# Performance work log

Hardware: AMD Instinct MI355X
Metric: run time of the kernel (lower is better)

The kernel has to match this reference:

```python
import jax, jax.numpy as jnp
import numpy as np

N_NODES = 50000
N_GENES = 256
N_EDGES = 800000
NUM_ITERATIONS = 10  # init_kwargs: num_iterations
SPARSITY = 0.3       # fraction of nonzero entries in expression matrix


def setup_inputs() -> dict:
    key = jax.random.key(0)
    k1, k2, k3, k4 = jax.random.split(key, 4)
    vals = jax.random.uniform(k1, (N_NODES, N_GENES), dtype=jnp.float32)
    keep = jax.random.uniform(k2, (N_NODES, N_GENES)) < SPARSITY
    x = jnp.where(keep, vals, 0.0)
    edge_index = jax.random.randint(k3, (2, N_EDGES), 0, N_NODES, dtype=jnp.int64)
    edge_weight = jax.random.uniform(k4, (N_EDGES,), dtype=jnp.float32)
    return {"x": x, "edge_index": edge_index, "edge_weight": edge_weight}


def reference(x, edge_index, edge_weight):
    # FeaturePropagation with mask=True, max_imputation_per_cell=None,
    # early_stopping=False: iterate x <- A @ x, then clamp known (nonzero)
    # entries back to their original values.
    n = x.shape[0]
    dst = edge_index[0]  # sparse COO row indices
    src = edge_index[1]  # sparse COO col indices
    orig = x
    known = x != 0

    def step(h, _):
        # SpMM: out[dst] += w * h[src]   (torch.sparse.mm(adj, x))
        msgs = edge_weight[:, None] * h[src]              # [E, G]
        h = jax.ops.segment_sum(msgs, dst, num_segments=n)  # [N, G]
        h = jnp.where(known, orig, h)  # reset known entries
        return h, None

    out, _ = jax.lax.scan(step, x, None, length=NUM_ITERATIONS)
    return out
```

## Files before the change

### kernel.cpp

```cpp
#include <hip/hip_runtime.h>

#define N_NODES 50000
#define N_GENES 256
#define N_EDGES 800000
#define NUM_ITERS 10
#define SCAN_BLK 1024
#define N_SCAN_BLKS ((N_NODES + SCAN_BLK - 1) / SCAN_BLK)

#define SLICE_G 128
#define N_SLICES 2
#define PROP_GRID 25000

typedef unsigned short u16;
struct u16x4 { u16 x, y, z, w; };

static __device__ __forceinline__ float bf2f(u16 b) {
    return __uint_as_float(((unsigned)b) << 16);
}
static __device__ __forceinline__ u16 f2bf(float f) {
    unsigned u = __float_as_uint(f);
    return (u16)((u + 0x7fffu + ((u >> 16) & 1u)) >> 16);
}


__global__ void hist_kernel(const int* __restrict__ dst, int* __restrict__ counts) {
    int e = blockIdx.x * blockDim.x + threadIdx.x;
    if (e < N_EDGES) atomicAdd(&counts[dst[e]], 1);
}

__global__ __launch_bounds__(SCAN_BLK) void scan1_kernel(
        const int* __restrict__ counts, int* __restrict__ offs,
        int* __restrict__ bsums) {
    int i = blockIdx.x * SCAN_BLK + threadIdx.x;
    int lane = threadIdx.x & 63, wid = threadIdx.x >> 6;
    int v = (i < N_NODES) ? counts[i] : 0;
    int x = v;
    #pragma unroll
    for (int o = 1; o < 64; o <<= 1) {
        int t = __shfl_up(x, o, 64);
        if (lane >= o) x += t;
    }
    __shared__ int wsum[16];
    if (lane == 63) wsum[wid] = x;
    __syncthreads();
    if (wid == 0 && lane < 16) {
        int y = wsum[lane];
        #pragma unroll
        for (int o = 1; o < 16; o <<= 1) {
            int t = __shfl_up(y, o, 64);
            if (lane >= o) y += t;
        }
        wsum[lane] = y;
    }
    __syncthreads();
    int pref = (wid > 0) ? wsum[wid - 1] : 0;
    int incl = x + pref;
    if (i < N_NODES) offs[i] = incl - v;
    if (threadIdx.x == SCAN_BLK - 1) bsums[blockIdx.x] = incl;
}

__global__ void scan2_kernel(const int* __restrict__ bsums,
                             int* __restrict__ bpref,
                             int* __restrict__ offs_total) {
    int lane = threadIdx.x;
    int v = (lane < N_SCAN_BLKS) ? bsums[lane] : 0;
    int x = v;
    #pragma unroll
    for (int o = 1; o < 64; o <<= 1) {
        int t = __shfl_up(x, o, 64);
        if (lane >= o) x += t;
    }
    if (lane < N_SCAN_BLKS) bpref[lane] = x - v;
    if (lane == 63) offs_total[0] = x;
}

__global__ __launch_bounds__(SCAN_BLK) void scan3_kernel(
        int* __restrict__ offs, const int* __restrict__ bpref,
        int* __restrict__ cursor) {
    int i = blockIdx.x * SCAN_BLK + threadIdx.x;
    if (i < N_NODES) {
        int o = offs[i] + bpref[blockIdx.x];
        offs[i] = o;
        cursor[i] = o;
    }
}

__global__ void scatter_kernel(const int* __restrict__ dst,
                               const int* __restrict__ src,
                               const float* __restrict__ w,
                               int* __restrict__ cursor,
                               int2* __restrict__ edges) {
    int e = blockIdx.x * blockDim.x + threadIdx.x;
    if (e < N_EDGES) {
        int d = dst[e];
        int p = atomicAdd(&cursor[d], 1);
        edges[p] = make_int2(src[e], __float_as_int(w[e]));
    }
}

__global__ __launch_bounds__(256) void cvt_slice_kernel(const float* __restrict__ x,
                                                        u16* __restrict__ xs) {
    int base = (blockIdx.x * blockDim.x + threadIdx.x) * 8;
    if (base >= N_NODES * N_GENES) return;
    int node = base >> 8;
    int gene = base & 255;
    int slice = gene >> 7;
    int g = gene & 127;
    float4 a = *reinterpret_cast<const float4*>(&x[base]);
    float4 b = *reinterpret_cast<const float4*>(&x[base + 4]);
    u16x4 r0 = { f2bf(a.x), f2bf(a.y), f2bf(a.z), f2bf(a.w) };
    u16x4 r1 = { f2bf(b.x), f2bf(b.y), f2bf(b.z), f2bf(b.w) };
    size_t o = (size_t)slice * (N_NODES * SLICE_G) + (size_t)node * SLICE_G + g;
    *reinterpret_cast<u16x4*>(&xs[o])     = r0;
    *reinterpret_cast<u16x4*>(&xs[o + 4]) = r1;
}


__global__ __launch_bounds__(256) void prop2_b(
        const u16* __restrict__ hin,
        const u16* __restrict__ xs,
        const int* __restrict__ offsets,
        const int2* __restrict__ edges,
        u16* __restrict__ out) {
    int b = blockIdx.x;
    int slice = ((b & 7) < 4) ? 0 : 1;
    int idx = (b >> 3) * 4 + (b & 3);
    int node = idx * 4 + (threadIdx.x >> 6);
    int lane = threadIdx.x & 63;
    int g2 = lane << 1;

    const u16* hs = hin + (size_t)slice * (N_NODES * SLICE_G);
    int beg = offsets[node], end = offsets[node + 1];
    float ax = 0.f, ay = 0.f;

    for (int base = beg; base < end; base += 64) {
        int cnt = end - base;
        if (cnt > 64) cnt = 64;
        int2 el = make_int2(0, 0);
        if (lane < cnt) {
            long long ev = __builtin_nontemporal_load(
                reinterpret_cast<const long long*>(&edges[base + lane]));
            el.x = (int)ev;
            el.y = (int)(ev >> 32);
        }

        int k = 0;
        for (; k + 8 <= cnt; k += 8) {
            int s[8]; float w[8]; unsigned p[8];
            #pragma unroll
            for (int j = 0; j < 8; ++j) {
                s[j] = __shfl(el.x, k + j);
                w[j] = __int_as_float(__shfl(el.y, k + j));
            }
            #pragma unroll
            for (int j = 0; j < 8; ++j)
                p[j] = *reinterpret_cast<const unsigned*>(&hs[(size_t)s[j] * SLICE_G + g2]);
            #pragma unroll
            for (int j = 0; j < 8; ++j) {
                ax += w[j] * bf2f((u16)p[j]);
                ay += w[j] * bf2f((u16)(p[j] >> 16));
            }
        }
        for (; k < cnt; ++k) {
            int   s = __shfl(el.x, k);
            float w = __int_as_float(__shfl(el.y, k));
            unsigned p = *reinterpret_cast<const unsigned*>(&hs[(size_t)s * SLICE_G + g2]);
            ax += w * bf2f((u16)p);
            ay += w * bf2f((u16)(p >> 16));
        }
    }

    size_t o = (size_t)slice * (N_NODES * SLICE_G) + (size_t)node * SLICE_G + g2;
    unsigned ox = __builtin_nontemporal_load(reinterpret_cast<const unsigned*>(&xs[o]));
    u16 b0 = (u16)(ox & 0xFFFFu), b1 = (u16)(ox >> 16);
    u16 r0 = b0 ? b0 : f2bf(ax);
    u16 r1 = b1 ? b1 : f2bf(ay);
    unsigned res = (unsigned)r0 | ((unsigned)r1 << 16);
    __builtin_nontemporal_store(res, reinterpret_cast<unsigned*>(&out[o]));
}

__global__ __launch_bounds__(256) void prop2_final(
        const u16* __restrict__ hin,
        const float* __restrict__ x,
        const int* __restrict__ offsets,
        const int2* __restrict__ edges,
        float* __restrict__ out) {
    int b = blockIdx.x;
    int slice = ((b & 7) < 4) ? 0 : 1;
    int idx = (b >> 3) * 4 + (b & 3);
    int node = idx * 4 + (threadIdx.x >> 6);
    int lane = threadIdx.x & 63;
    int g2 = lane << 1;

    const u16* hs = hin + (size_t)slice * (N_NODES * SLICE_G);
    int beg = offsets[node], end = offsets[node + 1];
    float ax = 0.f, ay = 0.f;

    for (int base = beg; base < end; base += 64) {
        int cnt = end - base;
        if (cnt > 64) cnt = 64;
        int2 el = make_int2(0, 0);
        if (lane < cnt) {
            long long ev = __builtin_nontemporal_load(
                reinterpret_cast<const long long*>(&edges[base + lane]));
            el.x = (int)ev;
            el.y = (int)(ev >> 32);
        }

        int k = 0;
        for (; k + 8 <= cnt; k += 8) {
            int s[8]; float w[8]; unsigned p[8];
            #pragma unroll
            for (int j = 0; j < 8; ++j) {
                s[j] = __shfl(el.x, k + j);
                w[j] = __int_as_float(__shfl(el.y, k + j));
            }
            #pragma unroll
            for (int j = 0; j < 8; ++j)
                p[j] = *reinterpret_cast<const unsigned*>(&hs[(size_t)s[j] * SLICE_G + g2]);
            #pragma unroll
            for (int j = 0; j < 8; ++j) {
                ax += w[j] * bf2f((u16)p[j]);
                ay += w[j] * bf2f((u16)(p[j] >> 16));
            }
        }
        for (; k < cnt; ++k) {
            int   s = __shfl(el.x, k);
            float w = __int_as_float(__shfl(el.y, k));
            unsigned p = *reinterpret_cast<const unsigned*>(&hs[(size_t)s * SLICE_G + g2]);
            ax += w * bf2f((u16)p);
            ay += w * bf2f((u16)(p >> 16));
        }
    }

    size_t xo = (size_t)node * N_GENES + slice * SLICE_G + g2;
    float2 o = *reinterpret_cast<const float2*>(&x[xo]);
    float2 r;
    r.x = (o.x != 0.f) ? o.x : ax;
    r.y = (o.y != 0.f) ? o.y : ay;
    *reinterpret_cast<float2*>(&out[xo]) = r;
}


static inline size_t align_up(size_t x, size_t a) { return (x + a - 1) & ~(a - 1); }

extern "C" void kernel_launch(void* const* d_in, const int* in_sizes, int n_in,
                              void* d_out, int out_size, void* d_ws, size_t ws_size,
                              hipStream_t stream) {
    const float* x    = (const float*)d_in[0];
    const int*   eidx = (const int*)d_in[1];
    const float* ew   = (const float*)d_in[2];
    float*       out  = (float*)d_out;

    const int* dst = eidx;
    const int* src = eidx + N_EDGES;

    char* ws = (char*)d_ws;
    size_t off = 0;
    u16*   xs      = (u16*) (ws + off); off += align_up((size_t)N_NODES * N_GENES * 2, 256);
    u16*   hsA     = (u16*) (ws + off); off += align_up((size_t)N_NODES * N_GENES * 2, 256);
    int2*  edges   = (int2*)(ws + off); off += align_up((size_t)N_EDGES * 8, 256);
    int*   counts  = (int*) (ws + off); off += align_up((size_t)N_NODES * 4, 256);
    int*   offsets = (int*) (ws + off); off += align_up((size_t)(N_NODES + 1) * 4, 256);
    int*   cursor  = (int*) (ws + off); off += align_up((size_t)N_NODES * 4, 256);
    int*   bsums   = (int*) (ws + off); off += align_up((size_t)N_SCAN_BLKS * 4, 256);
    int*   bpref   = (int*) (ws + off); off += align_up((size_t)N_SCAN_BLKS * 4, 256);
    (void)ws_size;

    u16* hsB = (u16*)d_out;

    hipMemsetAsync(counts, 0, (size_t)N_NODES * 4, stream);
    hist_kernel<<<(N_EDGES + 255) / 256, 256, 0, stream>>>(dst, counts);
    scan1_kernel<<<N_SCAN_BLKS, SCAN_BLK, 0, stream>>>(counts, offsets, bsums);
    scan2_kernel<<<1, 64, 0, stream>>>(bsums, bpref, &offsets[N_NODES]);
    scan3_kernel<<<N_SCAN_BLKS, SCAN_BLK, 0, stream>>>(offsets, bpref, cursor);
    scatter_kernel<<<(N_EDGES + 255) / 256, 256, 0, stream>>>(dst, src, ew, cursor, edges);
    cvt_slice_kernel<<<(N_NODES * N_GENES / 8 + 255) / 256, 256, 0, stream>>>(x, xs);

    const u16* hin = xs;
    for (int it = 0; it < NUM_ITERS - 1; ++it) {
        u16* hout = (it & 1) ? hsB : hsA;
        prop2_b<<<PROP_GRID, 256, 0, stream>>>(hin, xs, offsets, edges, hout);
        hin = hout;
    }
    prop2_final<<<PROP_GRID, 256, 0, stream>>>(hin, x, offsets, edges, out);
}
```

Before: 881.8 us.

## Split genes into eight 32-wide slices and pack edge metadata into 32 bits

After: 1.628 ms. 84.6% more time.

```diff
diff --git a/kernel.cpp b/kernel.cpp
--- a/kernel.cpp
+++ b/kernel.cpp
@@ -7,9 +7,9 @@
 #define SCAN_BLK 1024
 #define N_SCAN_BLKS ((N_NODES + SCAN_BLK - 1) / SCAN_BLK)
 
-#define SLICE_G 128
-#define N_SLICES 2
-#define PROP_GRID 25000
+#define SLICE_G 32
+#define N_SLICES 8
+#define PROP_GRID (12500 * 8)
 
 typedef unsigned short u16;
 struct u16x4 { u16 x, y, z, w; };
@@ -89,12 +89,12 @@
                                const int* __restrict__ src,
                                const float* __restrict__ w,
                                int* __restrict__ cursor,
-                               int2* __restrict__ edges) {
+                               unsigned* __restrict__ meta) {
     int e = blockIdx.x * blockDim.x + threadIdx.x;
     if (e < N_EDGES) {
         int d = dst[e];
         int p = atomicAdd(&cursor[d], 1);
-        edges[p] = make_int2(src[e], __float_as_int(w[e]));
+        meta[p] = (unsigned)(u16)src[e] | ((unsigned)f2bf(w[e]) << 16);
     }
 }
 
@@ -104,8 +104,8 @@
     if (base >= N_NODES * N_GENES) return;
     int node = base >> 8;
     int gene = base & 255;
-    int slice = gene >> 7;
-    int g = gene & 127;
+    int slice = gene >> 5;
+    int g = gene & 31;
     float4 a = *reinterpret_cast<const float4*>(&x[base]);
     float4 b = *reinterpret_cast<const float4*>(&x[base + 4]);
     u16x4 r0 = { f2bf(a.x), f2bf(a.y), f2bf(a.z), f2bf(a.w) };
@@ -116,129 +116,118 @@
 }
 
 
-__global__ __launch_bounds__(256) void prop2_b(
+__global__ __launch_bounds__(256) void prop8_b(
         const u16* __restrict__ hin,
         const u16* __restrict__ xs,
         const int* __restrict__ offsets,
-        const int2* __restrict__ edges,
+        const unsigned* __restrict__ meta,
         u16* __restrict__ out) {
-    int b = blockIdx.x;
-    int slice = ((b & 7) < 4) ? 0 : 1;
-    int idx = (b >> 3) * 4 + (b & 3);
-    int node = idx * 4 + (threadIdx.x >> 6);
+    int slice = blockIdx.x & 7;
+    int node  = (blockIdx.x >> 3) * 4 + (threadIdx.x >> 6);
     int lane = threadIdx.x & 63;
-    int g2 = lane << 1;
-
+    int sub = lane & 7;
+    int grp = lane >> 3;
     const u16* hs = hin + (size_t)slice * (N_NODES * SLICE_G);
+
     int beg = offsets[node], end = offsets[node + 1];
-    float ax = 0.f, ay = 0.f;
+    float a0 = 0.f, a1 = 0.f, a2 = 0.f, a3 = 0.f;
 
     for (int base = beg; base < end; base += 64) {
         int cnt = end - base;
         if (cnt > 64) cnt = 64;
-        int2 el = make_int2(0, 0);
-        if (lane < cnt) {
-            long long ev = __builtin_nontemporal_load(
-                reinterpret_cast<const long long*>(&edges[base + lane]));
-            el.x = (int)ev;
-            el.y = (int)(ev >> 32);
-        }
-
-        int k = 0;
-        for (; k + 8 <= cnt; k += 8) {
-            int s[8]; float w[8]; unsigned p[8];
-            #pragma unroll
-            for (int j = 0; j < 8; ++j) {
-                s[j] = __shfl(el.x, k + j);
-                w[j] = __int_as_float(__shfl(el.y, k + j));
-            }
-            #pragma unroll
-            for (int j = 0; j < 8; ++j)
-                p[j] = *reinterpret_cast<const unsigned*>(&hs[(size_t)s[j] * SLICE_G + g2]);
-            #pragma unroll
-            for (int j = 0; j < 8; ++j) {
-                ax += w[j] * bf2f((u16)p[j]);
-                ay += w[j] * bf2f((u16)(p[j] >> 16));
+        unsigned mv = 0;
+        if (lane < cnt) mv = __builtin_nontemporal_load(&meta[base + lane]);
+        int nb = (cnt + 7) >> 3;
+        for (int b = 0; b < nb; ++b) {
+            int eidx = b * 8 + grp;
+            unsigned m = __shfl(mv, eidx);
+            if (eidx < cnt) {
+                float w = bf2f((u16)(m >> 16));
+                int   s = (int)(m & 0xFFFFu);
+                u16x4 r = *reinterpret_cast<const u16x4*>(&hs[(size_t)s * SLICE_G + sub * 4]);
+                a0 += w * bf2f(r.x);
+                a1 += w * bf2f(r.y);
+                a2 += w * bf2f(r.z);
+                a3 += w * bf2f(r.w);
             }
         }
-        for (; k < cnt; ++k) {
-            int   s = __shfl(el.x, k);
-            float w = __int_as_float(__shfl(el.y, k));
-            unsigned p = *reinterpret_cast<const unsigned*>(&hs[(size_t)s * SLICE_G + g2]);
-            ax += w * bf2f((u16)p);
-            ay += w * bf2f((u16)(p >> 16));
-        }
-    }
-
-    size_t o = (size_t)slice * (N_NODES * SLICE_G) + (size_t)node * SLICE_G + g2;
-    unsigned ox = __builtin_nontemporal_load(reinterpret_cast<const unsigned*>(&xs[o]));
-    u16 b0 = (u16)(ox & 0xFFFFu), b1 = (u16)(ox >> 16);
-    u16 r0 = b0 ? b0 : f2bf(ax);
-    u16 r1 = b1 ? b1 : f2bf(ay);
-    unsigned res = (unsigned)r0 | ((unsigned)r1 << 16);
-    __builtin_nontemporal_store(res, reinterpret_cast<unsigned*>(&out[o]));
-}
-
-__global__ __launch_bounds__(256) void prop2_final(
+    }
+
+    #pragma unroll
+    for (int off = 8; off < 64; off <<= 1) {
+        a0 += __shfl_xor(a0, off);
+        a1 += __shfl_xor(a1, off);
+        a2 += __shfl_xor(a2, off);
+        a3 += __shfl_xor(a3, off);
+    }
+
+    if (grp == 0) {
+        size_t o = (size_t)slice * (N_NODES * SLICE_G) + (size_t)node * SLICE_G + sub * 4;
+        u16x4 ox = *reinterpret_cast<const u16x4*>(&xs[o]);
+        u16x4 res;
+        res.x = ox.x ? ox.x : f2bf(a0);
+        res.y = ox.y ? ox.y : f2bf(a1);
+        res.z = ox.z ? ox.z : f2bf(a2);
+        res.w = ox.w ? ox.w : f2bf(a3);
+        *reinterpret_cast<u16x4*>(&out[o]) = res;
+    }
+}
+
+__global__ __launch_bounds__(256) void prop8_final(
         const u16* __restrict__ hin,
         const float* __restrict__ x,
         const int* __restrict__ offsets,
-        const int2* __restrict__ edges,
+        const unsigned* __restrict__ meta,
         float* __restrict__ out) {
-    int b = blockIdx.x;
-    int slice = ((b & 7) < 4) ? 0 : 1;
-    int idx = (b >> 3) * 4 + (b & 3);
-    int node = idx * 4 + (threadIdx.x >> 6);
+    int slice = blockIdx.x & 7;
+    int node  = (blockIdx.x >> 3) * 4 + (threadIdx.x >> 6);
     int lane = threadIdx.x & 63;
-    int g2 = lane << 1;
-
+    int sub = lane & 7;
+    int grp = lane >> 3;
     const u16* hs = hin + (size_t)slice * (N_NODES * SLICE_G);
+
     int beg = offsets[node], end = offsets[node + 1];
-    float ax = 0.f, ay = 0.f;
+    float a0 = 0.f, a1 = 0.f, a2 = 0.f, a3 = 0.f;
 
     for (int base = beg; base < end; base += 64) {
         int cnt = end - base;
         if (cnt > 64) cnt = 64;
-        int2 el = make_int2(0, 0);
-        if (lane < cnt) {
-            long long ev = __builtin_nontemporal_load(
-                reinterpret_cast<const long long*>(&edges[base + lane]));
-            el.x = (int)ev;
-            el.y = (int)(ev >> 32);
-        }
-
-        int k = 0;
-        for (; k + 8 <= cnt; k += 8) {
-            int s[8]; float w[8]; unsigned p[8];
-            #pragma unroll
-            for (int j = 0; j < 8; ++j) {
-                s[j] = __shfl(el.x, k + j);
-                w[j] = __int_as_float(__shfl(el.y, k + j));
-            }
-            #pragma unroll
-            for (int j = 0; j < 8; ++j)
-                p[j] = *reinterpret_cast<const unsigned*>(&hs[(size_t)s[j] * SLICE_G + g2]);
-            #pragma unroll
-            for (int j = 0; j < 8; ++j) {
-                ax += w[j] * bf2f((u16)p[j]);
-                ay += w[j] * bf2f((u16)(p[j] >> 16));
+        unsigned mv = 0;
+        if (lane < cnt) mv = __builtin_nontemporal_load(&meta[base + lane]);
+        int nb = (cnt + 7) >> 3;
+        for (int b = 0; b < nb; ++b) {
+            int eidx = b * 8 + grp;
+            unsigned m = __shfl(mv, eidx);
+            if (eidx < cnt) {
+                float w = bf2f((u16)(m >> 16));
+                int   s = (int)(m & 0xFFFFu);
+                u16x4 r = *reinterpret_cast<const u16x4*>(&hs[(size_t)s * SLICE_G + sub * 4]);
+                a0 += w * bf2f(r.x);
+                a1 += w * bf2f(r.y);
+                a2 += w * bf2f(r.z);
+                a3 += w * bf2f(r.w);
             }
         }
-        for (; k < cnt; ++k) {
-            int   s = __shfl(el.x, k);
-            float w = __int_as_float(__shfl(el.y, k));
-            unsigned p = *reinterpret_cast<const unsigned*>(&hs[(size_t)s * SLICE_G + g2]);
-            ax += w * bf2f((u16)p);
-            ay += w * bf2f((u16)(p >> 16));
-        }
-    }
-
-    size_t xo = (size_t)node * N_GENES + slice * SLICE_G + g2;
-    float2 o = *reinterpret_cast<const float2*>(&x[xo]);
-    float2 r;
-    r.x = (o.x != 0.f) ? o.x : ax;
-    r.y = (o.y != 0.f) ? o.y : ay;
-    *reinterpret_cast<float2*>(&out[xo]) = r;
+    }
+
+    #pragma unroll
+    for (int off = 8; off < 64; off <<= 1) {
+        a0 += __shfl_xor(a0, off);
+        a1 += __shfl_xor(a1, off);
+        a2 += __shfl_xor(a2, off);
+        a3 += __shfl_xor(a3, off);
+    }
+
+    if (grp == 0) {
+        size_t xo = (size_t)node * N_GENES + slice * SLICE_G + sub * 4;
+        float4 o = *reinterpret_cast<const float4*>(&x[xo]);
+        float4 r;
+        r.x = (o.x != 0.f) ? o.x : a0;
+        r.y = (o.y != 0.f) ? o.y : a1;
+        r.z = (o.z != 0.f) ? o.z : a2;
+        r.w = (o.w != 0.f) ? o.w : a3;
+        *reinterpret_cast<float4*>(&out[xo]) = r;
+    }
 }
 
 
@@ -257,14 +246,14 @@
 
     char* ws = (char*)d_ws;
     size_t off = 0;
-    u16*   xs      = (u16*) (ws + off); off += align_up((size_t)N_NODES * N_GENES * 2, 256);
-    u16*   hsA     = (u16*) (ws + off); off += align_up((size_t)N_NODES * N_GENES * 2, 256);
-    int2*  edges   = (int2*)(ws + off); off += align_up((size_t)N_EDGES * 8, 256);
-    int*   counts  = (int*) (ws + off); off += align_up((size_t)N_NODES * 4, 256);
-    int*   offsets = (int*) (ws + off); off += align_up((size_t)(N_NODES + 1) * 4, 256);
-    int*   cursor  = (int*) (ws + off); off += align_up((size_t)N_NODES * 4, 256);
-    int*   bsums   = (int*) (ws + off); off += align_up((size_t)N_SCAN_BLKS * 4, 256);
-    int*   bpref   = (int*) (ws + off); off += align_up((size_t)N_SCAN_BLKS * 4, 256);
+    u16*      xs      = (u16*)     (ws + off); off += align_up((size_t)N_NODES * N_GENES * 2, 256);
+    u16*      hsA     = (u16*)     (ws + off); off += align_up((size_t)N_NODES * N_GENES * 2, 256);
+    unsigned* meta    = (unsigned*)(ws + off); off += align_up((size_t)N_EDGES * 4, 256);
+    int*      counts  = (int*)     (ws + off); off += align_up((size_t)N_NODES * 4, 256);
+    int*      offsets = (int*)     (ws + off); off += align_up((size_t)(N_NODES + 1) * 4, 256);
+    int*      cursor  = (int*)     (ws + off); off += align_up((size_t)N_NODES * 4, 256);
+    int*      bsums   = (int*)     (ws + off); off += align_up((size_t)N_SCAN_BLKS * 4, 256);
+    int*      bpref   = (int*)     (ws + off); off += align_up((size_t)N_SCAN_BLKS * 4, 256);
     (void)ws_size;
 
     u16* hsB = (u16*)d_out;
@@ -274,14 +263,14 @@
     scan1_kernel<<<N_SCAN_BLKS, SCAN_BLK, 0, stream>>>(counts, offsets, bsums);
     scan2_kernel<<<1, 64, 0, stream>>>(bsums, bpref, &offsets[N_NODES]);
     scan3_kernel<<<N_SCAN_BLKS, SCAN_BLK, 0, stream>>>(offsets, bpref, cursor);
-    scatter_kernel<<<(N_EDGES + 255) / 256, 256, 0, stream>>>(dst, src, ew, cursor, edges);
+    scatter_kernel<<<(N_EDGES + 255) / 256, 256, 0, stream>>>(dst, src, ew, cursor, meta);
     cvt_slice_kernel<<<(N_NODES * N_GENES / 8 + 255) / 256, 256, 0, stream>>>(x, xs);
 
     const u16* hin = xs;
     for (int it = 0; it < NUM_ITERS - 1; ++it) {
         u16* hout = (it & 1) ? hsB : hsA;
-        prop2_b<<<PROP_GRID, 256, 0, stream>>>(hin, xs, offsets, edges, hout);
+        prop8_b<<<PROP_GRID, 256, 0, stream>>>(hin, xs, offsets, meta, hout);
         hin = hout;
     }
-    prop2_final<<<PROP_GRID, 256, 0, stream>>>(hin, x, offsets, edges, out);
-}
+    prop8_final<<<PROP_GRID, 256, 0, stream>>>(hin, x, offsets, meta, out);
+}
```
